# Kernel optimization log

Hardware: AMD Instinct MI355X
Metric: run time of the kernel (lower is better)

The kernel has to match this reference:

```python
import jax, jax.numpy as jnp
import numpy as np

GAMMA = 0.99
LMBDA = 0.95


def setup_inputs() -> dict:
    key = jax.random.key(0)
    k1, k2, k3, k4 = jax.random.split(key, 4)
    B, T = 8192, 2048
    reward = jax.random.normal(k1, (B, T), dtype=jnp.float32)
    terminated = jax.random.randint(k2, (B, T), 0, 2).astype(jnp.bool_)
    value = jax.random.normal(k3, (B, T), dtype=jnp.float32)
    next_value = jax.random.normal(k4, (B, T), dtype=jnp.float32)
    return {"reward": reward, "terminated": terminated, "value": value, "next_value": next_value}


def reference(reward, terminated, value, next_value):
    # not_done: [B, T]
    not_done = 1.0 - terminated.astype(reward.dtype)
    # fake_bootstrap=False branch: zero out next_value at terminal steps
    delta = reward + GAMMA * (next_value * not_done) - value  # [B, T]
    coef = (GAMMA * LMBDA) * not_done                          # [B, T]

    def step(gae, xs):
        d_t, c_t = xs                 # each [B]
        gae = d_t + c_t * gae
        return gae, gae

    init = jnp.zeros(reward.shape[0], dtype=reward.dtype)
    # scan backward in time over [T, B] slices; reverse=True keeps outputs
    # aligned with the original time indices.
    _, adv_t = jax.lax.scan(step, init, (delta.T, coef.T), reverse=True)
    advantages = adv_t.T              # [B, T]
    returns = advantages + value
    return advantages, returns
```

## Files before the change

kernel.cpp:

```cpp
#include <hip/hip_runtime.h>


#define GAMMA 0.99f
#define LMBDA 0.95f

constexpr int T_LEN     = 2048;
constexpr int PER_THREAD = 8;
constexpr int BLOCK      = T_LEN / PER_THREAD;

__global__ __launch_bounds__(BLOCK) void gae_kernel(
    const float* __restrict__ reward,
    const int*   __restrict__ terminated,
    const float* __restrict__ value,
    const float* __restrict__ next_value,
    float* __restrict__ adv_out,
    float* __restrict__ ret_out)
{
    const int b   = blockIdx.x;
    const int j   = threadIdx.x;
    const size_t base = (size_t)b * T_LEN + (size_t)j * PER_THREAD;

    const float4* r4  = (const float4*)(reward     + base);
    const float4* v4  = (const float4*)(value      + base);
    const float4* n4  = (const float4*)(next_value + base);
    const int4*   t4  = (const int4*)  (terminated + base);

    float4 r0 = r4[0], r1 = r4[1];
    float4 v0 = v4[0], v1 = v4[1];
    float4 n0 = n4[0], n1 = n4[1];
    int4   tA = t4[0], tB = t4[1];

    float rr[8] = {r0.x, r0.y, r0.z, r0.w, r1.x, r1.y, r1.z, r1.w};
    float vv[8] = {v0.x, v0.y, v0.z, v0.w, v1.x, v1.y, v1.z, v1.w};
    float nn[8] = {n0.x, n0.y, n0.z, n0.w, n1.x, n1.y, n1.z, n1.w};
    int   tt[8] = {tA.x, tA.y, tA.z, tA.w, tB.x, tB.y, tB.z, tB.w};

    float delta[8], coef[8];
#pragma unroll
    for (int i = 0; i < 8; ++i) {
        float nd = tt[i] ? 0.0f : 1.0f;
        delta[i] = rr[i] + GAMMA * nn[i] * nd - vv[i];
        coef[i]  = (GAMMA * LMBDA) * nd;
    }

    float A = 0.0f, P = 1.0f;
#pragma unroll
    for (int i = 7; i >= 0; --i) {
        A = delta[i] + coef[i] * A;
        P = coef[i] * P;
    }

    const int lane = j & 63;
    const int wave = j >> 6;
    float SA = A, SP = P;
#pragma unroll
    for (int o = 1; o < 64; o <<= 1) {
        float A2 = __shfl_down(SA, o, 64);
        float P2 = __shfl_down(SP, o, 64);
        if (lane + o < 64) {
            SA = SA + SP * A2;
            SP = SP * P2;
        }
    }
    float EA = __shfl_down(SA, 1, 64);
    float EP = __shfl_down(SP, 1, 64);
    if (lane == 63) { EA = 0.0f; EP = 1.0f; }

    __shared__ float wA[BLOCK / 64];
    __shared__ float wP[BLOCK / 64];
    if (lane == 0) { wA[wave] = SA; wP[wave] = SP; }
    __syncthreads();

    float accA = 0.0f;
    for (int ww = (BLOCK / 64) - 1; ww > wave; --ww) {
        accA = wA[ww] + wP[ww] * accA;
    }

    float g = EA + EP * accA;

    float adv[8];
#pragma unroll
    for (int i = 7; i >= 0; --i) {
        g = delta[i] + coef[i] * g;
        adv[i] = g;
    }

    float4 a0 = {adv[0], adv[1], adv[2], adv[3]};
    float4 a1 = {adv[4], adv[5], adv[6], adv[7]};
    float4 q0 = {adv[0] + vv[0], adv[1] + vv[1], adv[2] + vv[2], adv[3] + vv[3]};
    float4 q1 = {adv[4] + vv[4], adv[5] + vv[5], adv[6] + vv[6], adv[7] + vv[7]};

    *(float4*)(adv_out + base)     = a0;
    *(float4*)(adv_out + base + 4) = a1;
    *(float4*)(ret_out + base)     = q0;
    *(float4*)(ret_out + base + 4) = q1;
}

extern "C" void kernel_launch(void* const* d_in, const int* in_sizes, int n_in,
                              void* d_out, int out_size, void* d_ws, size_t ws_size,
                              hipStream_t stream) {
    const float* reward     = (const float*)d_in[0];
    const int*   terminated = (const int*)  d_in[1];
    const float* value      = (const float*)d_in[2];
    const float* next_value = (const float*)d_in[3];

    const int total = in_sizes[0];
    const int B     = total / T_LEN;

    float* adv = (float*)d_out;
    float* ret = (float*)d_out + (size_t)total;

    gae_kernel<<<B, BLOCK, 0, stream>>>(reward, terminated, value, next_value, adv, ret);
}
```

Before: 316.9 us.

## Split each row into two halves for coalesced float4 access and nontemporal stores

Each thread now handles 4 contiguous elements in each of the two row halves instead of 8 contiguous elements, so every wave-wide float4 load and store is fully contiguous. The scan is restructured into two interleaved segment scans with a cross-half carry combined through shared memory. Outputs are written with nontemporal stores to reduce cache pollution. This adds a second set of shuffles and a somewhat more complex carry combination.

```diff
diff --git a/kernel.cpp b/kernel.cpp
--- a/kernel.cpp
+++ b/kernel.cpp
@@ -4,9 +4,11 @@
 #define GAMMA 0.99f
 #define LMBDA 0.95f
 
-constexpr int T_LEN     = 2048;
-constexpr int PER_THREAD = 8;
-constexpr int BLOCK      = T_LEN / PER_THREAD;
+constexpr int T_LEN = 2048;
+constexpr int BLOCK = 256;
+constexpr int HALF  = T_LEN / 2;
+
+typedef float v4f __attribute__((ext_vector_type(4)));
 
 __global__ __launch_bounds__(BLOCK) void gae_kernel(
     const float* __restrict__ reward,
@@ -16,84 +18,108 @@
     float* __restrict__ adv_out,
     float* __restrict__ ret_out)
 {
-    const int b   = blockIdx.x;
-    const int j   = threadIdx.x;
-    const size_t base = (size_t)b * T_LEN + (size_t)j * PER_THREAD;
+    const int b    = blockIdx.x;
+    const int j    = threadIdx.x;
+    const int lane = j & 63;
+    const int wave = j >> 6;
 
-    const float4* r4  = (const float4*)(reward     + base);
-    const float4* v4  = (const float4*)(value      + base);
-    const float4* n4  = (const float4*)(next_value + base);
-    const int4*   t4  = (const int4*)  (terminated + base);
+    const size_t row   = (size_t)b * T_LEN;
+    const size_t base0 = row + (size_t)4 * j;
+    const size_t base1 = row + HALF + (size_t)4 * j;
 
-    float4 r0 = r4[0], r1 = r4[1];
-    float4 v0 = v4[0], v1 = v4[1];
-    float4 n0 = n4[0], n1 = n4[1];
-    int4   tA = t4[0], tB = t4[1];
+    float4 r0 = *(const float4*)(reward     + base0);
+    float4 r1 = *(const float4*)(reward     + base1);
+    float4 v0 = *(const float4*)(value      + base0);
+    float4 v1 = *(const float4*)(value      + base1);
+    float4 n0 = *(const float4*)(next_value + base0);
+    float4 n1 = *(const float4*)(next_value + base1);
+    int4   t0 = *(const int4*)  (terminated + base0);
+    int4   t1 = *(const int4*)  (terminated + base1);
 
-    float rr[8] = {r0.x, r0.y, r0.z, r0.w, r1.x, r1.y, r1.z, r1.w};
-    float vv[8] = {v0.x, v0.y, v0.z, v0.w, v1.x, v1.y, v1.z, v1.w};
-    float nn[8] = {n0.x, n0.y, n0.z, n0.w, n1.x, n1.y, n1.z, n1.w};
-    int   tt[8] = {tA.x, tA.y, tA.z, tA.w, tB.x, tB.y, tB.z, tB.w};
-
-    float delta[8], coef[8];
+    float d0[4], c0[4], d1[4], c1[4];
+    float vv0[4] = {v0.x, v0.y, v0.z, v0.w};
+    float vv1[4] = {v1.x, v1.y, v1.z, v1.w};
+    {
+        float rr0[4] = {r0.x, r0.y, r0.z, r0.w};
+        float nn0[4] = {n0.x, n0.y, n0.z, n0.w};
+        int   tt0[4] = {t0.x, t0.y, t0.z, t0.w};
+        float rr1[4] = {r1.x, r1.y, r1.z, r1.w};
+        float nn1[4] = {n1.x, n1.y, n1.z, n1.w};
+        int   tt1[4] = {t1.x, t1.y, t1.z, t1.w};
 #pragma unroll
-    for (int i = 0; i < 8; ++i) {
-        float nd = tt[i] ? 0.0f : 1.0f;
-        delta[i] = rr[i] + GAMMA * nn[i] * nd - vv[i];
-        coef[i]  = (GAMMA * LMBDA) * nd;
+        for (int i = 0; i < 4; ++i) {
+            float nd0 = tt0[i] ? 0.0f : 1.0f;
+            float nd1 = tt1[i] ? 0.0f : 1.0f;
+            d0[i] = rr0[i] + GAMMA * nn0[i] * nd0 - vv0[i];
+            c0[i] = (GAMMA * LMBDA) * nd0;
+            d1[i] = rr1[i] + GAMMA * nn1[i] * nd1 - vv1[i];
+            c1[i] = (GAMMA * LMBDA) * nd1;
+        }
     }
 
-    float A = 0.0f, P = 1.0f;
+    float A0 = 0.0f, P0 = 1.0f, A1 = 0.0f, P1 = 1.0f;
 #pragma unroll
-    for (int i = 7; i >= 0; --i) {
-        A = delta[i] + coef[i] * A;
-        P = coef[i] * P;
+    for (int i = 3; i >= 0; --i) {
+        A0 = d0[i] + c0[i] * A0;  P0 = c0[i] * P0;
+        A1 = d1[i] + c1[i] * A1;  P1 = c1[i] * P1;
     }
 
-    const int lane = j & 63;
-    const int wave = j >> 6;
-    float SA = A, SP = P;
+    float SA0 = A0, SP0 = P0, SA1 = A1, SP1 = P1;
 #pragma unroll
     for (int o = 1; o < 64; o <<= 1) {
-        float A2 = __shfl_down(SA, o, 64);
-        float P2 = __shfl_down(SP, o, 64);
+        float tA0 = __shfl_down(SA0, o, 64);
+        float tP0 = __shfl_down(SP0, o, 64);
+        float tA1 = __shfl_down(SA1, o, 64);
+        float tP1 = __shfl_down(SP1, o, 64);
         if (lane + o < 64) {
-            SA = SA + SP * A2;
-            SP = SP * P2;
+            SA0 = SA0 + SP0 * tA0;  SP0 = SP0 * tP0;
+            SA1 = SA1 + SP1 * tA1;  SP1 = SP1 * tP1;
         }
     }
-    float EA = __shfl_down(SA, 1, 64);
-    float EP = __shfl_down(SP, 1, 64);
-    if (lane == 63) { EA = 0.0f; EP = 1.0f; }
+    float EA0 = __shfl_down(SA0, 1, 64);
+    float EP0 = __shfl_down(SP0, 1, 64);
+    float EA1 = __shfl_down(SA1, 1, 64);
+    float EP1 = __shfl_down(SP1, 1, 64);
+    if (lane == 63) { EA0 = 0.0f; EP0 = 1.0f; EA1 = 0.0f; EP1 = 1.0f; }
 
-    __shared__ float wA[BLOCK / 64];
-    __shared__ float wP[BLOCK / 64];
-    if (lane == 0) { wA[wave] = SA; wP[wave] = SP; }
+    __shared__ float wA0[4], wP0[4], wA1[4], wP1[4];
+    if (lane == 0) { wA0[wave] = SA0; wP0[wave] = SP0; wA1[wave] = SA1; wP1[wave] = SP1; }
     __syncthreads();
 
-    float accA = 0.0f;
-    for (int ww = (BLOCK / 64) - 1; ww > wave; --ww) {
-        accA = wA[ww] + wP[ww] * accA;
+    float acc1A = 0.0f;
+    float acc0A = 0.0f, acc0P = 1.0f;
+    float full1 = 0.0f;
+#pragma unroll
+    for (int ww = 3; ww >= 0; --ww) {
+        if (ww > wave) {
+            acc1A = wA1[ww] + wP1[ww] * acc1A;
+            acc0A = wA0[ww] + wP0[ww] * acc0A;
+            acc0P = wP0[ww] * acc0P;
+        }
+        full1 = wA1[ww] + wP1[ww] * full1;
     }
 
-    float g = EA + EP * accA;
+    float g1_in = EA1 + EP1 * acc1A;
+    float g_mid = full1;
+    float g0_in = EA0 + EP0 * (acc0A + acc0P * g_mid);
 
-    float adv[8];
+    float a1[4], a0[4];
+    float g = g1_in;
 #pragma unroll
-    for (int i = 7; i >= 0; --i) {
-        g = delta[i] + coef[i] * g;
-        adv[i] = g;
-    }
+    for (int i = 3; i >= 0; --i) { g = d1[i] + c1[i] * g; a1[i] = g; }
+    g = g0_in;
+#pragma unroll
+    for (int i = 3; i >= 0; --i) { g = d0[i] + c0[i] * g; a0[i] = g; }
 
-    float4 a0 = {adv[0], adv[1], adv[2], adv[3]};
-    float4 a1 = {adv[4], adv[5], adv[6], adv[7]};
-    float4 q0 = {adv[0] + vv[0], adv[1] + vv[1], adv[2] + vv[2], adv[3] + vv[3]};
-    float4 q1 = {adv[4] + vv[4], adv[5] + vv[5], adv[6] + vv[6], adv[7] + vv[7]};
+    v4f adv0 = {a0[0], a0[1], a0[2], a0[3]};
+    v4f adv1 = {a1[0], a1[1], a1[2], a1[3]};
+    v4f ret0 = {a0[0] + vv0[0], a0[1] + vv0[1], a0[2] + vv0[2], a0[3] + vv0[3]};
+    v4f ret1 = {a1[0] + vv1[0], a1[1] + vv1[1], a1[2] + vv1[2], a1[3] + vv1[3]};
 
-    *(float4*)(adv_out + base)     = a0;
-    *(float4*)(adv_out + base + 4) = a1;
-    *(float4*)(ret_out + base)     = q0;
-    *(float4*)(ret_out + base + 4) = q1;
+    __builtin_nontemporal_store(adv0, (v4f*)(adv_out + base0));
+    __builtin_nontemporal_store(adv1, (v4f*)(adv_out + base1));
+    __builtin_nontemporal_store(ret0, (v4f*)(ret_out + base0));
+    __builtin_nontemporal_store(ret1, (v4f*)(ret_out + base1));
 }
 
 extern "C" void kernel_launch(void* const* d_in, const int* in_sizes, int n_in,
```

Result: slower. 324.4 us (+2.4%).
